# Optimization experiments

Measured on AMD Instinct MI355X. Metric: run time of the kernel, lower is better.

Reference implementation:

```python
import jax, jax.numpy as jnp
import numpy as np

N_NODES = 100000
N_EDGES = 1600000


def gcn_conv(x, W, b, src, dst, ew, n):
    """PyG GCNConv: x@W, symmetric deg^-1/2 norm with self-loops, scatter-add at dst, +b."""
    loop = jnp.arange(n, dtype=src.dtype)
    s = jnp.concatenate([src, loop])            # sources incl. self-loops
    d = jnp.concatenate([dst, loop])            # targets incl. self-loops
    w = jnp.concatenate([ew, jnp.ones((n,), ew.dtype)])  # self-loop weight = 1
    deg = jax.ops.segment_sum(w, d, num_segments=n)      # weighted in-degree
    dinv = jnp.where(deg > 0, jax.lax.rsqrt(deg), 0.0)
    norm = dinv[s] * w * dinv[d]                # [E+N]
    h = x @ W                                   # [N, F_out]
    msg = h[s] * norm[:, None]                  # gather + per-edge scale
    out = jax.ops.segment_sum(msg, d, num_segments=n)    # scatter-add
    return out + b


def setup_inputs() -> dict:
    key = jax.random.key(0)
    ks = jax.random.split(key, 8)
    in_dim, hid, lat = 128, 128, 64
    x = jax.random.normal(ks[0], (N_NODES, in_dim), jnp.float32)
    edge_index = jax.random.randint(ks[1], (2, N_EDGES), 0, N_NODES, dtype=jnp.int32)
    weights = jax.random.uniform(ks[2], (N_EDGES,), jnp.float32)
    s_in = 1.0 / np.sqrt(in_dim)
    s_h = 1.0 / np.sqrt(hid)
    return {
        "x": x,
        "edge_index": edge_index,
        "weights": weights,
        "W1": jax.random.normal(ks[3], (in_dim, hid), jnp.float32) * s_in,
        "b1": jnp.zeros((hid,), jnp.float32),
        "W2": jax.random.normal(ks[4], (hid, hid), jnp.float32) * s_h,
        "b2": jnp.zeros((hid,), jnp.float32),
        "W_mu": jax.random.normal(ks[5], (hid, lat), jnp.float32) * s_h,
        "b_mu": jnp.zeros((lat,), jnp.float32),
        "W_lv": jax.random.normal(ks[6], (hid, lat), jnp.float32) * s_h,
        "b_lv": jnp.zeros((lat,), jnp.float32),
    }


def reference(x, edge_index, weights, W1, b1, W2, b2, W_mu, b_mu, W_lv, b_lv):
    n = x.shape[0]
    src, dst = edge_index[0], edge_index[1]
    h = jax.nn.relu(gcn_conv(x, W1, b1, src, dst, weights, n))
    h = gcn_conv(h, W2, b2, src, dst, weights, n)
    g = jnp.mean(h, axis=0, keepdims=True)      # [1, hid] global mean pool
    mu = g @ W_mu + b_mu
    logvar = g @ W_lv + b_lv
    return (mu, logvar)
```

## Files before the change

### kernel.cpp

```cpp
#include <hip/hip_runtime.h>


typedef __bf16 bf16x8 __attribute__((ext_vector_type(8)));
typedef float f32x4 __attribute__((ext_vector_type(4)));
typedef float f32x2 __attribute__((ext_vector_type(2)));
typedef unsigned long long u64;

#define NSL 24

__device__ __forceinline__ float bf2f(unsigned short u){
  return __uint_as_float(((unsigned)u) << 16);
}
__device__ __forceinline__ unsigned short f2bf(float f){
  unsigned u = __float_as_uint(f);
  u += 0x7fffu + ((u >> 16) & 1u);
  return (unsigned short)(u >> 16);
}
__device__ __forceinline__ __bf16 us2bf(unsigned short u){
  __bf16 b; __builtin_memcpy(&b, &u, 2); return b;
}
__device__ __forceinline__ float ldf(const void* p, int i, int isf32){
  return isf32 ? ((const float*)p)[i] : bf2f(((const unsigned short*)p)[i]);
}
__device__ __forceinline__ void fma8f8(float* acc, float n, uint2 h){
  f32x2 p0 = __builtin_amdgcn_cvt_pk_f32_fp8((int)h.x, false);
  f32x2 p1 = __builtin_amdgcn_cvt_pk_f32_fp8((int)h.x, true);
  f32x2 p2 = __builtin_amdgcn_cvt_pk_f32_fp8((int)h.y, false);
  f32x2 p3 = __builtin_amdgcn_cvt_pk_f32_fp8((int)h.y, true);
  acc[0] = fmaf(n, p0[0], acc[0]);
  acc[1] = fmaf(n, p0[1], acc[1]);
  acc[2] = fmaf(n, p1[0], acc[2]);
  acc[3] = fmaf(n, p1[1], acc[3]);
  acc[4] = fmaf(n, p2[0], acc[4]);
  acc[5] = fmaf(n, p2[1], acc[5]);
  acc[6] = fmaf(n, p3[0], acc[6]);
  acc[7] = fmaf(n, p3[1], acc[7]);
}
__device__ __forceinline__ void runOfShard(const int* __restrict__ hist, int r, int s,
                                           int lane, int& off, int& len){
  int hv = (lane < 8) ? hist[r * 8 + lane] : 0;
  off = 0; len = 0;
  #pragma unroll
  for (int i = 0; i < 8; ++i){
    int h = __shfl(hv, i);
    if (i < s) off += h;
    if (i == s) len = h;
  }
}

__global__ void k_init(const unsigned* __restrict__ xw, int* __restrict__ flag,
                       const void* __restrict__ W1, unsigned short* __restrict__ W1T,
                       float* __restrict__ v){
  __shared__ int s[256];
  int t = threadIdx.x;
  int cnt = 0;
  for (int k = t; k < 4096; k += 256){
    unsigned lo = xw[k] & 0xFFFFu;
    int e = (int)((lo >> 7) & 0xFFu);
    if ((e >= 100 && e <= 141) || (lo & 0x7FFFu) == 0) cnt++;
  }
  s[t] = cnt;
  __syncthreads();
  for (int off = 128; off > 0; off >>= 1){
    if (t < off) s[t] += s[t + off];
    __syncthreads();
  }
  int isf32 = (s[0] < 2458) ? 1 : 0;
  if (blockIdx.x == 0){
    if (t == 0) *flag = isf32;
    if (t < 128) v[t] = 0.0f;
  }
  int gid = blockIdx.x * 256 + t;
  int k = gid & 127, n = gid >> 7;
  W1T[gid] = isf32 ? f2bf(((const float*)W1)[k * 128 + n])
                   : ((const unsigned short*)W1)[k * 128 + n];
}

__global__ void __launch_bounds__(256) k_binA(const int* __restrict__ src,
    const int* __restrict__ dst, const void* __restrict__ w,
    u64* __restrict__ stagD, u64* __restrict__ stagS,
    int* __restrict__ histD, int* __restrict__ histS,
    int E, int DSv, const int* __restrict__ flagp){
  __shared__ int gcnt[256];
  __shared__ int gincl[256];
  __shared__ u64 bufD[1024];
  __shared__ u64 bufS[1024];
  int tid = threadIdx.x, lane = tid & 63, wv = tid >> 6;
  gcnt[tid] = 0;
  __syncthreads();
  int isf32 = *flagp;
  u64 ltmask = (1ull << lane) - 1ull;
  int sh1v[4], off1v[4], sh2v[4], off2v[4];
  u64 r1v[4], r2v[4];
  #pragma unroll
  for (int k = 0; k < 4; ++k){
    int e = blockIdx.x * 1024 + k * 256 + tid;
    int sh1 = -1, sh2 = -1; u64 r1 = 0, r2 = 0;
    if (e < E){
      int s_ = src[e], d_ = dst[e];
      float wf = ldf(w, e, isf32);
      int nq = (int)(wf * 32768.0f + 0.5f);
      if (nq > 32767) nq = 32767;
      r1 = ((u64)(unsigned)d_ << 32) | ((u64)(unsigned)s_ << 15) | (unsigned)nq;
      r2 = ((u64)(unsigned)s_ << 32) | ((u64)(unsigned)d_ << 15) | (unsigned)nq;
      sh1 = d_ / DSv;
      sh2 = s_ / DSv;
    }
    int o1 = 0, o2 = 0;
    #pragma unroll
    for (int s = 0; s < 8; ++s){
      u64 m1 = __ballot(sh1 == s);
      if (sh1 == s){ o1 = __popcll(m1 & ltmask); if (!o1) gcnt[s * 16 + k * 4 + wv] = __popcll(m1); }
      u64 m2 = __ballot(sh2 == s);
      if (sh2 == s){ o2 = __popcll(m2 & ltmask); if (!o2) gcnt[128 + s * 16 + k * 4 + wv] = __popcll(m2); }
    }
    sh1v[k] = sh1; off1v[k] = o1; r1v[k] = r1;
    sh2v[k] = sh2; off2v[k] = o2; r2v[k] = r2;
  }
  __syncthreads();
  gincl[tid] = gcnt[tid];
  __syncthreads();
  for (int ofs = 1; ofs < 256; ofs <<= 1){
    int t2 = (tid >= ofs) ? gincl[tid - ofs] : 0;
    __syncthreads();
    gincl[tid] += t2;
    __syncthreads();
  }
  int tot1 = gincl[127];
  #pragma unroll
  for (int k = 0; k < 4; ++k){
    if (sh1v[k] >= 0){
      int i1 = sh1v[k] * 16 + k * 4 + wv;
      bufD[gincl[i1] - gcnt[i1] + off1v[k]] = r1v[k];
      int i2 = 128 + sh2v[k] * 16 + k * 4 + wv;
      bufS[gincl[i2] - gcnt[i2] - tot1 + off2v[k]] = r2v[k];
    }
  }
  __syncthreads();
  for (int t = tid; t < tot1; t += 256)
    stagD[(size_t)blockIdx.x * 1024 + t] = bufD[t];
  int tot2 = gincl[255] - tot1;
  for (int t = tid; t < tot2; t += 256)
    stagS[(size_t)blockIdx.x * 1024 + t] = bufS[t];
  if (tid < 8){
    int a  = gincl[tid * 16 + 15];
    int pr = tid ? gincl[tid * 16 - 1] : 0;
    histD[blockIdx.x * 8 + tid] = a - pr;
    int a2  = gincl[128 + tid * 16 + 15];
    int pr2 = gincl[128 + tid * 16 - 1];
    histS[blockIdx.x * 8 + tid] = a2 - pr2;
  }
}

__global__ void __launch_bounds__(256) k_binB(const u64* __restrict__ stagD,
    const int* __restrict__ histD, unsigned* __restrict__ cntdegP,
    int NREG, int per, int DSv){
  __shared__ unsigned cd[12512];
  int tid = threadIdx.x, lane = tid & 63, wv = tid >> 6;
  int s = (int)blockIdx.x & 7, j = (int)blockIdx.x >> 3;
  for (int i = tid; i < DSv; i += 256) cd[i] = 0u;
  __syncthreads();
  int r0 = j * per, r1 = r0 + per;
  if (r1 > NREG) r1 = NREG;
  for (int r = r0 + wv; r < r1; r += 4){
    int off, len;
    runOfShard(histD, r, s, lane, off, len);
    const u64* rp = stagD + (size_t)r * 1024 + off;
    for (int i = lane; i < len; i += 64){
      u64 rec = rp[i];
      int dl = (int)(rec >> 32) - s * DSv;
      if ((unsigned)dl < (unsigned)DSv)
        atomicAdd(&cd[dl], (1u << 20) | (unsigned)((rec & 32767u) >> 2));
    }
  }
  __syncthreads();
  unsigned* op = cntdegP + (size_t)blockIdx.x * DSv;
  for (int i = tid; i < DSv; i += 256) op[i] = cd[i];
}

__global__ void k_scanA(const unsigned* __restrict__ cntdegP, float* __restrict__ dinv,
                        int* __restrict__ cnt, int* __restrict__ rowptr,
                        int* __restrict__ bsum, int N, int DSv){
  __shared__ int sm[256];
  int i = blockIdx.x * 256 + threadIdx.x;
  int val = 0;
  if (i < N){
    int s = i / DSv, local = i - s * DSv;
    unsigned c = 0, dg = 0;
    #pragma unroll
    for (int j = 0; j < NSL; ++j){
      unsigned p = cntdegP[(size_t)(j * 8 + s) * DSv + local];
      c += p >> 20;
      dg += p & 0xFFFFFu;
    }
    dinv[i] = rsqrtf(1.0f + (float)dg * (1.0f / 8192.0f));
    cnt[i] = (int)c;
    val = (int)c;
  }
  sm[threadIdx.x] = val;
  __syncthreads();
  for (int off = 1; off < 256; off <<= 1){
    int tmp = (threadIdx.x >= off) ? sm[threadIdx.x - off] : 0;
    __syncthreads();
    sm[threadIdx.x] += tmp;
    __syncthreads();
  }
  if (i < N) rowptr[i] = sm[threadIdx.x] - val;
  if (threadIdx.x == 255) bsum[blockIdx.x] = sm[255];
}

__global__ void k_scanB(const int* __restrict__ bsum, int* __restrict__ boffs, int NB){
  __shared__ int s[512];
  int t = threadIdx.x;
  int val = (t < NB) ? bsum[t] : 0;
  s[t] = val;
  __syncthreads();
  for (int off = 1; off < 512; off <<= 1){
    int tmp = (t >= off) ? s[t - off] : 0;
    __syncthreads();
    s[t] += tmp;
    __syncthreads();
  }
  boffs[t] = s[t] - val;
}

__global__ void k_scanC(int* __restrict__ rowptr, const int* __restrict__ boffs,
                        const unsigned* __restrict__ cntdegP, int* __restrict__ P,
                        int N, int DSv){
  int i = blockIdx.x * 256 + threadIdx.x;
  if (i >= N) return;
  int rp = rowptr[i] + boffs[blockIdx.x];
  rowptr[i] = rp;
  int s = i / DSv, local = i - s * DSv;
  int run = rp;
  #pragma unroll
  for (int j = 0; j < NSL; ++j){
    P[(size_t)j * N + i] = run;
    run += (int)(cntdegP[(size_t)(j * 8 + s) * DSv + local] >> 20);
  }
}

__global__ void __launch_bounds__(256) k_binC(const u64* __restrict__ stagD,
    const int* __restrict__ histD, const int* __restrict__ P,
    const float* __restrict__ dinv, unsigned* __restrict__ edges,
    int NREG, int per, int N, int DSv, int E){
  __shared__ unsigned cur[12512];
  int tid = threadIdx.x, lane = tid & 63, wv = tid >> 6;
  int s = (int)blockIdx.x & 7, j = (int)blockIdx.x >> 3;
  for (int i = tid; i < DSv; i += 256){
    int node = s * DSv + i;
    cur[i] = (node < N) ? (unsigned)P[(size_t)j * N + node] : 0u;
  }
  __syncthreads();
  int r0 = j * per, r1 = r0 + per;
  if (r1 > NREG) r1 = NREG;
  for (int r = r0 + wv; r < r1; r += 4){
    int off, len;
    runOfShard(histD, r, s, lane, off, len);
    const u64* rp = stagD + (size_t)r * 1024 + off;
    for (int i = lane; i < len; i += 64){
      u64 rec = rp[i];
      int dl = (int)(rec >> 32) - s * DSv;
      if ((unsigned)dl < (unsigned)DSv){
        int srcI = (int)((rec >> 15) & 0x1FFFFu);
        float nrm = dinv[srcI] * ((float)(rec & 32767u) * (1.0f / 32768.0f))
                  * dinv[s * DSv + dl];
        int nq = (int)(nrm * 32768.0f + 0.5f);
        if (nq > 32767) nq = 32767;
        unsigned pos = atomicAdd(&cur[dl], 1u);
        if (pos < (unsigned)E) edges[pos] = ((unsigned)srcI << 15) | (unsigned)nq;
      }
    }
  }
}

__global__ void __launch_bounds__(256) k_cfacB(const u64* __restrict__ stagS,
    const int* __restrict__ histS, const float* __restrict__ dinv,
    float* __restrict__ cfacP, int NREG, int per, int DSv){
  __shared__ float SL[12512];
  int tid = threadIdx.x, lane = tid & 63, wv = tid >> 6;
  int s = (int)blockIdx.x & 7, j = (int)blockIdx.x >> 3;
  for (int i = tid; i < DSv; i += 256) SL[i] = 0.0f;
  __syncthreads();
  int r0 = j * per, r1 = r0 + per;
  if (r1 > NREG) r1 = NREG;
  for (int r = r0 + wv; r < r1; r += 4){
    int off, len;
    runOfShard(histS, r, s, lane, off, len);
    const u64* rp = stagS + (size_t)r * 1024 + off;
    for (int i = lane; i < len; i += 64){
      u64 rec = rp[i];
      int sl_ = (int)(rec >> 32) - s * DSv;
      int d   = (int)((rec >> 15) & 0x1FFFFu);
      float wq = (float)(rec & 32767u) * (1.0f / 32768.0f);
      if ((unsigned)sl_ < (unsigned)DSv)
        atomicAdd(&SL[sl_], wq * dinv[d]);
    }
  }
  __syncthreads();
  float* op = cfacP + (size_t)blockIdx.x * DSv;
  for (int i = tid; i < DSv; i += 256) op[i] = SL[i];
}

__global__ void k_cfacm(const float* __restrict__ cfacP, const float* __restrict__ dinv,
                        const int* __restrict__ rowptr, const int* __restrict__ cnt,
                        float2* __restrict__ dc, int2* __restrict__ rc,
                        unsigned* __restrict__ edges, int E, int N, int DSv){
  if (blockIdx.x == 0 && threadIdx.x < 16) edges[E + threadIdx.x] = 0u;
  int i = blockIdx.x * 256 + threadIdx.x;
  if (i >= N) return;
  int s = i / DSv, ii = i - s * DSv;
  float S = 0.0f;
  #pragma unroll
  for (int j = 0; j < NSL; ++j)
    S += cfacP[(size_t)(j * 8 + s) * DSv + ii];
  float di = dinv[i];
  dc[i] = make_float2(di * di, di * di + di * S);
  rc[i] = make_int2(rowptr[i], cnt[i]);
}

__global__ void __launch_bounds__(256) k_gemm(const void* __restrict__ xv,
                                              const __bf16* __restrict__ wt,
                                              unsigned char* __restrict__ H, int N,
                                              const int* __restrict__ flagp){
  int wave = (blockIdx.x * blockDim.x + threadIdx.x) >> 6;
  int lane = threadIdx.x & 63;
  int row16 = wave << 4;
  if (row16 >= N) return;
  int isf32 = *flagp;
  int m = lane & 15, q = lane >> 4;
  bf16x8 a0, a1, a2, a3;
  if (isf32){
    const float* ap = (const float*)xv + (size_t)(row16 + m) * 128 + q * 8;
    #pragma unroll
    for (int j = 0; j < 8; ++j){
      a0[j] = us2bf(f2bf(ap[j +  0]));
      a1[j] = us2bf(f2bf(ap[j + 32]));
      a2[j] = us2bf(f2bf(ap[j + 64]));
      a3[j] = us2bf(f2bf(ap[j + 96]));
    }
  } else {
    const __bf16* ap = (const __bf16*)xv + (size_t)(row16 + m) * 128 + q * 8;
    a0 = *(const bf16x8*)(ap +  0);
    a1 = *(const bf16x8*)(ap + 32);
    a2 = *(const bf16x8*)(ap + 64);
    a3 = *(const bf16x8*)(ap + 96);
  }
  for (int nt = 0; nt < 8; ++nt){
    const __bf16* bp = wt + (size_t)(nt * 16 + m) * 128 + q * 8;
    bf16x8 b0 = *(const bf16x8*)(bp +  0);
    bf16x8 b1 = *(const bf16x8*)(bp + 32);
    bf16x8 b2 = *(const bf16x8*)(bp + 64);
    bf16x8 b3 = *(const bf16x8*)(bp + 96);
    f32x4 acc = {0.f, 0.f, 0.f, 0.f};
    acc = __builtin_amdgcn_mfma_f32_16x16x32_bf16(a0, b0, acc, 0, 0, 0);
    acc = __builtin_amdgcn_mfma_f32_16x16x32_bf16(a1, b1, acc, 0, 0, 0);
    acc = __builtin_amdgcn_mfma_f32_16x16x32_bf16(a2, b2, acc, 0, 0, 0);
    acc = __builtin_amdgcn_mfma_f32_16x16x32_bf16(a3, b3, acc, 0, 0, 0);
    unsigned char* op = H + (size_t)(row16 + q * 4) * 128 + nt * 16 + m;
    op[0]   = (unsigned char)(__builtin_amdgcn_cvt_pk_fp8_f32(acc[0], acc[0], 0, false) & 0xFF);
    op[128] = (unsigned char)(__builtin_amdgcn_cvt_pk_fp8_f32(acc[1], acc[1], 0, false) & 0xFF);
    op[256] = (unsigned char)(__builtin_amdgcn_cvt_pk_fp8_f32(acc[2], acc[2], 0, false) & 0xFF);
    op[384] = (unsigned char)(__builtin_amdgcn_cvt_pk_fp8_f32(acc[3], acc[3], 0, false) & 0xFF);
  }
}

__global__ void __launch_bounds__(256) k_agg(const unsigned char* __restrict__ H,
    const int2* __restrict__ rc, const float2* __restrict__ dc,
    const unsigned* __restrict__ edges, const void* __restrict__ b1,
    float* __restrict__ v, int N, int totslots, const int* __restrict__ flagp){
  __shared__ float vsh[128];
  __shared__ float bsh[128];
  int tid = threadIdx.x;
  int isf32 = *flagp;
  if (tid < 128){ vsh[tid] = 0.0f; bsh[tid] = ldf(b1, tid, isf32); }
  __syncthreads();
  int lane = tid & 63;
  int wv = tid >> 6;
  int slot = lane >> 3;
  int q = lane & 7;
  int slotg = ((int)blockIdx.x * 4 + wv) * 8 + slot;
  const unsigned char* Hq = H + q * 16;
  float ax[16];
  #pragma unroll
  for (int j = 0; j < 16; ++j) ax[j] = 0.0f;
  int d = slotg;
  int2 rcv = make_int2(0, 0); float2 dcv = make_float2(0.f, 0.f);
  uint4 hs = make_uint4(0u, 0u, 0u, 0u);
  if (d < N){
    rcv = rc[d]; dcv = dc[d];
    hs = *(const uint4*)(Hq + (size_t)d * 128);
  }
  while (d < N){
    int dn = d + totslots;
    int2 rcn = make_int2(0, 0); float2 dcn = make_float2(0.f, 0.f);
    uint4 hsn = make_uint4(0u, 0u, 0u, 0u);
    if (dn < N){
      rcn = rc[dn]; dcn = dc[dn];
      hsn = *(const uint4*)(Hq + (size_t)dn * 128);
    }
    float acc[16];
    #pragma unroll
    for (int j = 0; j < 16; ++j) acc[j] = 0.0f;
    fma8f8(acc,     dcv.x, make_uint2(hs.x, hs.y));
    fma8f8(acc + 8, dcv.x, make_uint2(hs.z, hs.w));
    int start = rcv.x, len = rcv.y;
    if (len > 0){
      const unsigned* ep = edges + start;
      unsigned e0 = ep[0], e1 = ep[1], e2 = ep[2], e3 = ep[3];
      uint4 h0 = *(const uint4*)(Hq + (size_t)(e0 >> 15) * 128);
      uint4 h1 = *(const uint4*)(Hq + (size_t)(e1 >> 15) * 128);
      uint4 h2 = *(const uint4*)(Hq + (size_t)(e2 >> 15) * 128);
      #pragma unroll 2
      for (int k = 0; k < len; ++k){
        unsigned en = ep[k + 4];
        uint4 hn = *(const uint4*)(Hq + (size_t)(e3 >> 15) * 128);
        float wn = (float)(e0 & 32767u) * (1.0f / 32768.0f);
        fma8f8(acc,     wn, make_uint2(h0.x, h0.y));
        fma8f8(acc + 8, wn, make_uint2(h0.z, h0.w));
        e0 = e1; e1 = e2; e2 = e3; e3 = en;
        h0 = h1; h1 = h2; h2 = hn;
      }
    }
    #pragma unroll
    for (int j = 0; j < 16; ++j){
      float rj = fmaxf(acc[j] + bsh[q * 16 + j], 0.0f);
      ax[j] = fmaf(dcv.y, rj, ax[j]);
    }
    d = dn; rcv = rcn; dcv = dcn; hs = hsn;
  }
  #pragma unroll
  for (int j = 0; j < 16; ++j){
    ax[j] += __shfl_xor(ax[j], 8);
    ax[j] += __shfl_xor(ax[j], 16);
    ax[j] += __shfl_xor(ax[j], 32);
  }
  if (slot == 0){
    #pragma unroll
    for (int j = 0; j < 16; ++j) atomicAdd(&vsh[q * 16 + j], ax[j]);
  }
  __syncthreads();
  if (tid < 128) atomicAdd(&v[tid], vsh[tid]);
}

__global__ void __launch_bounds__(128) k_head(const float* __restrict__ v,
    const void* __restrict__ W2, const void* __restrict__ b2,
    const void* __restrict__ Wmu, const void* __restrict__ bmu,
    const void* __restrict__ Wlv, const void* __restrict__ blv,
    void* __restrict__ outv, float invN, const int* __restrict__ flagp){
  __shared__ float gsh[128];
  __shared__ float tsh[128];
  int t = threadIdx.x;
  int isf32 = *flagp;
  gsh[t] = v[t] * invN;
  __syncthreads();
  float acc = ldf(b2, t, isf32);
  for (int k = 0; k < 128; ++k) acc = fmaf(gsh[k], ldf(W2, k * 128 + t, isf32), acc);
  tsh[t] = acc;
  __syncthreads();
  int j = t & 63;
  const void* Wp = (t < 64) ? Wmu : Wlv;
  float o = ldf((t < 64) ? bmu : blv, j, isf32);
  for (int k = 0; k < 128; ++k) o = fmaf(tsh[k], ldf(Wp, k * 64 + j, isf32), o);
  if (isf32) ((float*)outv)[t] = o;
  else       ((unsigned short*)outv)[t] = f2bf(o);
}

extern "C" void kernel_launch(void* const* d_in, const int* in_sizes, int n_in,
                              void* d_out, int out_size, void* d_ws, size_t ws_size,
                              hipStream_t stream) {
  const void* x   = d_in[0];
  const int*  ei  = (const int*)d_in[1];
  const void* w   = d_in[2];
  const void* W1  = d_in[3];
  const void* b1  = d_in[4];
  const void* W2  = d_in[5];
  const void* b2  = d_in[6];
  const void* Wmu = d_in[7];
  const void* bmu = d_in[8];
  const void* Wlv = d_in[9];
  const void* blv = d_in[10];

  const int N = in_sizes[0] / 128;
  const int E = in_sizes[2];
  const int* src = ei;
  const int* dst = ei + E;

  char* wsb = (char*)d_ws;
  size_t off = 0;
  auto alloc = [&](size_t bytes) -> void* {
    off = (off + 255) & ~(size_t)255;
    void* p = wsb + off;
    off += bytes;
    return p;
  };
  const int NREG = (E + 1023) / 1024;
  const int PER  = (NREG + NSL - 1) / NSL;
  const int DSv  = (N + 7) / 8;
  int*   flag     = (int*)  alloc(16);
  float* dinv     = (float*)alloc((size_t)N * 4);
  int*   cnt      = (int*)  alloc((size_t)N * 4);
  int*   rowptr   = (int*)  alloc((size_t)(N + 1) * 4);
  float2* dc      = (float2*)alloc((size_t)N * 8);
  int2*   rc      = (int2*) alloc((size_t)N * 8);
  int*   bsum     = (int*)  alloc(512 * 4);
  int*   boffs    = (int*)  alloc(512 * 4);
  float* v        = (float*)alloc(128 * 4);
  int*   histD    = (int*)  alloc((size_t)NREG * 8 * 4);
  int*   histS    = (int*)  alloc((size_t)NREG * 8 * 4);
  unsigned short* W1T = (unsigned short*)alloc(128 * 128 * 2);
  size_t P_b = (size_t)NSL * N * 4, cfacP_b = (size_t)NSL * 8 * DSv * 4;
  char* regionP = (char*)alloc(P_b > cfacP_b ? P_b : cfacP_b);
  int*   P     = (int*)regionP;
  float* cfacP = (float*)regionP;
  size_t cdg_b = (size_t)NSL * 8 * DSv * 4, edges_b = (size_t)E * 4 + 64;
  char* regionE = (char*)alloc(cdg_b > edges_b ? cdg_b : edges_b);
  unsigned* cntdegP = (unsigned*)regionE;
  unsigned* edges   = (unsigned*)regionE;
  size_t stagD_b = (size_t)NREG * 1024 * 8, H_b = (size_t)N * 128;
  char* regionD = (char*)alloc(stagD_b > H_b ? stagD_b : H_b);
  u64*           stagD = (u64*)regionD;
  unsigned char* H     = (unsigned char*)regionD;
  u64* stagS = (u64*)alloc((size_t)NREG * 1024 * 8);
  (void)ws_size; (void)n_in; (void)out_size;

  const int nb_n = (N + 255) / 256;

  k_init<<<64, 256, 0, stream>>>((const unsigned*)x, flag, W1, W1T, v);
  k_binA<<<NREG, 256, 0, stream>>>(src, dst, w, stagD, stagS, histD, histS,
                                   E, DSv, flag);
  k_binB<<<NSL * 8, 256, 0, stream>>>(stagD, histD, cntdegP, NREG, PER, DSv);
  k_scanA<<<nb_n, 256, 0, stream>>>(cntdegP, dinv, cnt, rowptr, bsum, N, DSv);
  k_scanB<<<1, 512, 0, stream>>>(bsum, boffs, nb_n);
  k_scanC<<<nb_n, 256, 0, stream>>>(rowptr, boffs, cntdegP, P, N, DSv);
  k_binC<<<NSL * 8, 256, 0, stream>>>(stagD, histD, P, dinv, edges,
                                      NREG, PER, N, DSv, E);
  k_cfacB<<<NSL * 8, 256, 0, stream>>>(stagS, histS, dinv, cfacP, NREG, PER, DSv);
  k_cfacm<<<nb_n, 256, 0, stream>>>(cfacP, dinv, rowptr, cnt, dc, rc,
                                    edges, E, N, DSv);
  const int nwaves = (N + 15) / 16;
  const int nb_g = (nwaves + 3) / 4;
  k_gemm<<<nb_g, 256, 0, stream>>>(x, (const __bf16*)W1T, H, N, flag);
  const int nb_agg = 1024;
  k_agg<<<nb_agg, 256, 0, stream>>>(H, rc, dc, edges, b1, v, N, nb_agg * 32, flag);
  k_head<<<1, 128, 0, stream>>>(v, W2, b2, Wmu, bmu, Wlv, blv,
                                d_out, 1.0f / (float)N, flag);
}
```

Measured before the change: 374.6 us.

## Replace shard-binned CSR build with direct global-atomic degree and edge scatter

Drops the multi-pass staging pipeline (per-block shard binning, LDS-histogram partial counts, per-slice prefix offsets) and builds the CSR with plain global atomics. One 64-bit atomic per edge packs the count and the quantized weighted degree, and a second kernel places each edge with an atomic cursor and accumulates the source-side column factor with a float atomic. This removes several kernels and large staging buffers. In exchange it relies on contended global atomics with random access, and the order of edges within a row becomes nondeterministic.

```diff
diff --git a/kernel.cpp b/kernel.cpp
--- a/kernel.cpp
+++ b/kernel.cpp
@@ -5,8 +5,6 @@
 typedef float f32x4 __attribute__((ext_vector_type(4)));
 typedef float f32x2 __attribute__((ext_vector_type(2)));
 typedef unsigned long long u64;
-
-#define NSL 24
 
 __device__ __forceinline__ float bf2f(unsigned short u){
   return __uint_as_float(((unsigned)u) << 16);
@@ -36,21 +34,10 @@
   acc[6] = fmaf(n, p3[0], acc[6]);
   acc[7] = fmaf(n, p3[1], acc[7]);
 }
-__device__ __forceinline__ void runOfShard(const int* __restrict__ hist, int r, int s,
-                                           int lane, int& off, int& len){
-  int hv = (lane < 8) ? hist[r * 8 + lane] : 0;
-  off = 0; len = 0;
-  #pragma unroll
-  for (int i = 0; i < 8; ++i){
-    int h = __shfl(hv, i);
-    if (i < s) off += h;
-    if (i == s) len = h;
-  }
-}
 
 __global__ void k_init(const unsigned* __restrict__ xw, int* __restrict__ flag,
                        const void* __restrict__ W1, unsigned short* __restrict__ W1T,
-                       float* __restrict__ v){
+                       float* __restrict__ v, u64* __restrict__ degcnt, int N){
   __shared__ int s[256];
   int t = threadIdx.x;
   int cnt = 0;
@@ -71,131 +58,39 @@
     if (t < 128) v[t] = 0.0f;
   }
   int gid = blockIdx.x * 256 + t;
+  for (int i = gid; i < N; i += 16384) degcnt[i] = 0ull;
   int k = gid & 127, n = gid >> 7;
   W1T[gid] = isf32 ? f2bf(((const float*)W1)[k * 128 + n])
                    : ((const unsigned short*)W1)[k * 128 + n];
 }
 
-__global__ void __launch_bounds__(256) k_binA(const int* __restrict__ src,
-    const int* __restrict__ dst, const void* __restrict__ w,
-    u64* __restrict__ stagD, u64* __restrict__ stagS,
-    int* __restrict__ histD, int* __restrict__ histS,
-    int E, int DSv, const int* __restrict__ flagp){
-  __shared__ int gcnt[256];
-  __shared__ int gincl[256];
-  __shared__ u64 bufD[1024];
-  __shared__ u64 bufS[1024];
-  int tid = threadIdx.x, lane = tid & 63, wv = tid >> 6;
-  gcnt[tid] = 0;
-  __syncthreads();
-  int isf32 = *flagp;
-  u64 ltmask = (1ull << lane) - 1ull;
-  int sh1v[4], off1v[4], sh2v[4], off2v[4];
-  u64 r1v[4], r2v[4];
-  #pragma unroll
-  for (int k = 0; k < 4; ++k){
-    int e = blockIdx.x * 1024 + k * 256 + tid;
-    int sh1 = -1, sh2 = -1; u64 r1 = 0, r2 = 0;
-    if (e < E){
-      int s_ = src[e], d_ = dst[e];
-      float wf = ldf(w, e, isf32);
-      int nq = (int)(wf * 32768.0f + 0.5f);
-      if (nq > 32767) nq = 32767;
-      r1 = ((u64)(unsigned)d_ << 32) | ((u64)(unsigned)s_ << 15) | (unsigned)nq;
-      r2 = ((u64)(unsigned)s_ << 32) | ((u64)(unsigned)d_ << 15) | (unsigned)nq;
-      sh1 = d_ / DSv;
-      sh2 = s_ / DSv;
-    }
-    int o1 = 0, o2 = 0;
-    #pragma unroll
-    for (int s = 0; s < 8; ++s){
-      u64 m1 = __ballot(sh1 == s);
-      if (sh1 == s){ o1 = __popcll(m1 & ltmask); if (!o1) gcnt[s * 16 + k * 4 + wv] = __popcll(m1); }
-      u64 m2 = __ballot(sh2 == s);
-      if (sh2 == s){ o2 = __popcll(m2 & ltmask); if (!o2) gcnt[128 + s * 16 + k * 4 + wv] = __popcll(m2); }
-    }
-    sh1v[k] = sh1; off1v[k] = o1; r1v[k] = r1;
-    sh2v[k] = sh2; off2v[k] = o2; r2v[k] = r2;
-  }
-  __syncthreads();
-  gincl[tid] = gcnt[tid];
-  __syncthreads();
-  for (int ofs = 1; ofs < 256; ofs <<= 1){
-    int t2 = (tid >= ofs) ? gincl[tid - ofs] : 0;
-    __syncthreads();
-    gincl[tid] += t2;
-    __syncthreads();
-  }
-  int tot1 = gincl[127];
-  #pragma unroll
-  for (int k = 0; k < 4; ++k){
-    if (sh1v[k] >= 0){
-      int i1 = sh1v[k] * 16 + k * 4 + wv;
-      bufD[gincl[i1] - gcnt[i1] + off1v[k]] = r1v[k];
-      int i2 = 128 + sh2v[k] * 16 + k * 4 + wv;
-      bufS[gincl[i2] - gcnt[i2] - tot1 + off2v[k]] = r2v[k];
-    }
-  }
-  __syncthreads();
-  for (int t = tid; t < tot1; t += 256)
-    stagD[(size_t)blockIdx.x * 1024 + t] = bufD[t];
-  int tot2 = gincl[255] - tot1;
-  for (int t = tid; t < tot2; t += 256)
-    stagS[(size_t)blockIdx.x * 1024 + t] = bufS[t];
-  if (tid < 8){
-    int a  = gincl[tid * 16 + 15];
-    int pr = tid ? gincl[tid * 16 - 1] : 0;
-    histD[blockIdx.x * 8 + tid] = a - pr;
-    int a2  = gincl[128 + tid * 16 + 15];
-    int pr2 = gincl[128 + tid * 16 - 1];
-    histS[blockIdx.x * 8 + tid] = a2 - pr2;
-  }
-}
-
-__global__ void __launch_bounds__(256) k_binB(const u64* __restrict__ stagD,
-    const int* __restrict__ histD, unsigned* __restrict__ cntdegP,
-    int NREG, int per, int DSv){
-  __shared__ unsigned cd[12512];
-  int tid = threadIdx.x, lane = tid & 63, wv = tid >> 6;
-  int s = (int)blockIdx.x & 7, j = (int)blockIdx.x >> 3;
-  for (int i = tid; i < DSv; i += 256) cd[i] = 0u;
-  __syncthreads();
-  int r0 = j * per, r1 = r0 + per;
-  if (r1 > NREG) r1 = NREG;
-  for (int r = r0 + wv; r < r1; r += 4){
-    int off, len;
-    runOfShard(histD, r, s, lane, off, len);
-    const u64* rp = stagD + (size_t)r * 1024 + off;
-    for (int i = lane; i < len; i += 64){
-      u64 rec = rp[i];
-      int dl = (int)(rec >> 32) - s * DSv;
-      if ((unsigned)dl < (unsigned)DSv)
-        atomicAdd(&cd[dl], (1u << 20) | (unsigned)((rec & 32767u) >> 2));
-    }
-  }
-  __syncthreads();
-  unsigned* op = cntdegP + (size_t)blockIdx.x * DSv;
-  for (int i = tid; i < DSv; i += 256) op[i] = cd[i];
-}
-
-__global__ void k_scanA(const unsigned* __restrict__ cntdegP, float* __restrict__ dinv,
+__global__ void __launch_bounds__(256) k_deg(const int* __restrict__ dst,
+    const void* __restrict__ w, u64* __restrict__ degcnt, int E,
+    const int* __restrict__ flagp){
+  int isf32 = *flagp;
+  int e = blockIdx.x * 256 + threadIdx.x;
+  if (e >= E) return;
+  int d_ = dst[e];
+  float wf = ldf(w, e, isf32);
+  int nq = (int)(wf * 32768.0f + 0.5f);
+  if (nq > 32767) nq = 32767;
+  atomicAdd(&degcnt[d_], (1ull << 40) | (u64)(unsigned)(nq >> 2));
+}
+
+__global__ void k_scanA(const u64* __restrict__ degcnt, float* __restrict__ dinv,
                         int* __restrict__ cnt, int* __restrict__ rowptr,
-                        int* __restrict__ bsum, int N, int DSv){
+                        int* __restrict__ bsum, float* __restrict__ S, int N){
   __shared__ int sm[256];
   int i = blockIdx.x * 256 + threadIdx.x;
   int val = 0;
   if (i < N){
-    int s = i / DSv, local = i - s * DSv;
-    unsigned c = 0, dg = 0;
-    #pragma unroll
-    for (int j = 0; j < NSL; ++j){
-      unsigned p = cntdegP[(size_t)(j * 8 + s) * DSv + local];
-      c += p >> 20;
-      dg += p & 0xFFFFFu;
-    }
+    u64 p = degcnt[i];
+    u64 dg = p & ((1ull << 40) - 1ull);
+    int c = (int)(p >> 40);
     dinv[i] = rsqrtf(1.0f + (float)dg * (1.0f / 8192.0f));
-    cnt[i] = (int)c;
-    val = (int)c;
+    cnt[i] = c;
+    val = c;
+    S[i] = 0.0f;
   }
   sm[threadIdx.x] = val;
   __syncthreads();
@@ -225,97 +120,45 @@
 }
 
 __global__ void k_scanC(int* __restrict__ rowptr, const int* __restrict__ boffs,
-                        const unsigned* __restrict__ cntdegP, int* __restrict__ P,
-                        int N, int DSv){
+                        unsigned* __restrict__ cur, int N){
   int i = blockIdx.x * 256 + threadIdx.x;
   if (i >= N) return;
   int rp = rowptr[i] + boffs[blockIdx.x];
   rowptr[i] = rp;
-  int s = i / DSv, local = i - s * DSv;
-  int run = rp;
-  #pragma unroll
-  for (int j = 0; j < NSL; ++j){
-    P[(size_t)j * N + i] = run;
-    run += (int)(cntdegP[(size_t)(j * 8 + s) * DSv + local] >> 20);
-  }
-}
-
-__global__ void __launch_bounds__(256) k_binC(const u64* __restrict__ stagD,
-    const int* __restrict__ histD, const int* __restrict__ P,
-    const float* __restrict__ dinv, unsigned* __restrict__ edges,
-    int NREG, int per, int N, int DSv, int E){
-  __shared__ unsigned cur[12512];
-  int tid = threadIdx.x, lane = tid & 63, wv = tid >> 6;
-  int s = (int)blockIdx.x & 7, j = (int)blockIdx.x >> 3;
-  for (int i = tid; i < DSv; i += 256){
-    int node = s * DSv + i;
-    cur[i] = (node < N) ? (unsigned)P[(size_t)j * N + node] : 0u;
-  }
-  __syncthreads();
-  int r0 = j * per, r1 = r0 + per;
-  if (r1 > NREG) r1 = NREG;
-  for (int r = r0 + wv; r < r1; r += 4){
-    int off, len;
-    runOfShard(histD, r, s, lane, off, len);
-    const u64* rp = stagD + (size_t)r * 1024 + off;
-    for (int i = lane; i < len; i += 64){
-      u64 rec = rp[i];
-      int dl = (int)(rec >> 32) - s * DSv;
-      if ((unsigned)dl < (unsigned)DSv){
-        int srcI = (int)((rec >> 15) & 0x1FFFFu);
-        float nrm = dinv[srcI] * ((float)(rec & 32767u) * (1.0f / 32768.0f))
-                  * dinv[s * DSv + dl];
-        int nq = (int)(nrm * 32768.0f + 0.5f);
-        if (nq > 32767) nq = 32767;
-        unsigned pos = atomicAdd(&cur[dl], 1u);
-        if (pos < (unsigned)E) edges[pos] = ((unsigned)srcI << 15) | (unsigned)nq;
-      }
-    }
-  }
-}
-
-__global__ void __launch_bounds__(256) k_cfacB(const u64* __restrict__ stagS,
-    const int* __restrict__ histS, const float* __restrict__ dinv,
-    float* __restrict__ cfacP, int NREG, int per, int DSv){
-  __shared__ float SL[12512];
-  int tid = threadIdx.x, lane = tid & 63, wv = tid >> 6;
-  int s = (int)blockIdx.x & 7, j = (int)blockIdx.x >> 3;
-  for (int i = tid; i < DSv; i += 256) SL[i] = 0.0f;
-  __syncthreads();
-  int r0 = j * per, r1 = r0 + per;
-  if (r1 > NREG) r1 = NREG;
-  for (int r = r0 + wv; r < r1; r += 4){
-    int off, len;
-    runOfShard(histS, r, s, lane, off, len);
-    const u64* rp = stagS + (size_t)r * 1024 + off;
-    for (int i = lane; i < len; i += 64){
-      u64 rec = rp[i];
-      int sl_ = (int)(rec >> 32) - s * DSv;
-      int d   = (int)((rec >> 15) & 0x1FFFFu);
-      float wq = (float)(rec & 32767u) * (1.0f / 32768.0f);
-      if ((unsigned)sl_ < (unsigned)DSv)
-        atomicAdd(&SL[sl_], wq * dinv[d]);
-    }
-  }
-  __syncthreads();
-  float* op = cfacP + (size_t)blockIdx.x * DSv;
-  for (int i = tid; i < DSv; i += 256) op[i] = SL[i];
-}
-
-__global__ void k_cfacm(const float* __restrict__ cfacP, const float* __restrict__ dinv,
+  cur[i] = (unsigned)rp;
+}
+
+__global__ void __launch_bounds__(256) k_edges(const int* __restrict__ src,
+    const int* __restrict__ dst, const void* __restrict__ w,
+    const float* __restrict__ dinv, unsigned* __restrict__ cur,
+    float* __restrict__ S, unsigned* __restrict__ edges, int E,
+    const int* __restrict__ flagp){
+  int isf32 = *flagp;
+  int e = blockIdx.x * 256 + threadIdx.x;
+  if (e >= E) return;
+  int s_ = src[e], d_ = dst[e];
+  float wf = ldf(w, e, isf32);
+  int wq = (int)(wf * 32768.0f + 0.5f);
+  if (wq > 32767) wq = 32767;
+  float wqf = (float)wq * (1.0f / 32768.0f);
+  float dd = dinv[d_];
+  float nrm = dinv[s_] * wqf * dd;
+  int nq = (int)(nrm * 32768.0f + 0.5f);
+  if (nq > 32767) nq = 32767;
+  unsigned pos = atomicAdd(&cur[d_], 1u);
+  edges[pos] = ((unsigned)s_ << 15) | (unsigned)nq;
+  atomicAdd(&S[s_], wqf * dd);
+}
+
+__global__ void k_cfacm(const float* __restrict__ S, const float* __restrict__ dinv,
                         const int* __restrict__ rowptr, const int* __restrict__ cnt,
                         float2* __restrict__ dc, int2* __restrict__ rc,
-                        unsigned* __restrict__ edges, int E, int N, int DSv){
+                        unsigned* __restrict__ edges, int E, int N){
   if (blockIdx.x == 0 && threadIdx.x < 16) edges[E + threadIdx.x] = 0u;
   int i = blockIdx.x * 256 + threadIdx.x;
   if (i >= N) return;
-  int s = i / DSv, ii = i - s * DSv;
-  float S = 0.0f;
-  #pragma unroll
-  for (int j = 0; j < NSL; ++j)
-    S += cfacP[(size_t)(j * 8 + s) * DSv + ii];
   float di = dinv[i];
-  dc[i] = make_float2(di * di, di * di + di * S);
+  dc[i] = make_float2(di * di, di * di + di * S[i]);
   rc[i] = make_int2(rowptr[i], cnt[i]);
 }
 
@@ -379,12 +222,11 @@
   int wv = tid >> 6;
   int slot = lane >> 3;
   int q = lane & 7;
-  int slotg = ((int)blockIdx.x * 4 + wv) * 8 + slot;
   const unsigned char* Hq = H + q * 16;
   float ax[16];
   #pragma unroll
   for (int j = 0; j < 16; ++j) ax[j] = 0.0f;
-  int d = slotg;
+  int d = ((int)blockIdx.x * 4 + wv) * 8 + slot;
   int2 rcv = make_int2(0, 0); float2 dcv = make_float2(0.f, 0.f);
   uint4 hs = make_uint4(0u, 0u, 0u, 0u);
   if (d < N){
@@ -494,9 +336,6 @@
     off += bytes;
     return p;
   };
-  const int NREG = (E + 1023) / 1024;
-  const int PER  = (NREG + NSL - 1) / NSL;
-  const int DSv  = (N + 7) / 8;
   int*   flag     = (int*)  alloc(16);
   float* dinv     = (float*)alloc((size_t)N * 4);
   int*   cnt      = (int*)  alloc((size_t)N * 4);
@@ -506,38 +345,24 @@
   int*   bsum     = (int*)  alloc(512 * 4);
   int*   boffs    = (int*)  alloc(512 * 4);
   float* v        = (float*)alloc(128 * 4);
-  int*   histD    = (int*)  alloc((size_t)NREG * 8 * 4);
-  int*   histS    = (int*)  alloc((size_t)NREG * 8 * 4);
   unsigned short* W1T = (unsigned short*)alloc(128 * 128 * 2);
-  size_t P_b = (size_t)NSL * N * 4, cfacP_b = (size_t)NSL * 8 * DSv * 4;
-  char* regionP = (char*)alloc(P_b > cfacP_b ? P_b : cfacP_b);
-  int*   P     = (int*)regionP;
-  float* cfacP = (float*)regionP;
-  size_t cdg_b = (size_t)NSL * 8 * DSv * 4, edges_b = (size_t)E * 4 + 64;
-  char* regionE = (char*)alloc(cdg_b > edges_b ? cdg_b : edges_b);
-  unsigned* cntdegP = (unsigned*)regionE;
-  unsigned* edges   = (unsigned*)regionE;
-  size_t stagD_b = (size_t)NREG * 1024 * 8, H_b = (size_t)N * 128;
-  char* regionD = (char*)alloc(stagD_b > H_b ? stagD_b : H_b);
-  u64*           stagD = (u64*)regionD;
-  unsigned char* H     = (unsigned char*)regionD;
-  u64* stagS = (u64*)alloc((size_t)NREG * 1024 * 8);
+  u64*      degcnt = (u64*)     alloc((size_t)N * 8);
+  unsigned* cur    = (unsigned*)alloc((size_t)N * 4);
+  float*    S      = (float*)   alloc((size_t)N * 4);
+  unsigned* edges  = (unsigned*)alloc((size_t)E * 4 + 64);
+  unsigned char* H = (unsigned char*)alloc((size_t)N * 128);
   (void)ws_size; (void)n_in; (void)out_size;
 
   const int nb_n = (N + 255) / 256;
-
-  k_init<<<64, 256, 0, stream>>>((const unsigned*)x, flag, W1, W1T, v);
-  k_binA<<<NREG, 256, 0, stream>>>(src, dst, w, stagD, stagS, histD, histS,
-                                   E, DSv, flag);
-  k_binB<<<NSL * 8, 256, 0, stream>>>(stagD, histD, cntdegP, NREG, PER, DSv);
-  k_scanA<<<nb_n, 256, 0, stream>>>(cntdegP, dinv, cnt, rowptr, bsum, N, DSv);
+  const int nb_e = (E + 255) / 256;
+
+  k_init<<<64, 256, 0, stream>>>((const unsigned*)x, flag, W1, W1T, v, degcnt, N);
+  k_deg<<<nb_e, 256, 0, stream>>>(dst, w, degcnt, E, flag);
+  k_scanA<<<nb_n, 256, 0, stream>>>(degcnt, dinv, cnt, rowptr, bsum, S, N);
   k_scanB<<<1, 512, 0, stream>>>(bsum, boffs, nb_n);
-  k_scanC<<<nb_n, 256, 0, stream>>>(rowptr, boffs, cntdegP, P, N, DSv);
-  k_binC<<<NSL * 8, 256, 0, stream>>>(stagD, histD, P, dinv, edges,
-                                      NREG, PER, N, DSv, E);
-  k_cfacB<<<NSL * 8, 256, 0, stream>>>(stagS, histS, dinv, cfacP, NREG, PER, DSv);
-  k_cfacm<<<nb_n, 256, 0, stream>>>(cfacP, dinv, rowptr, cnt, dc, rc,
-                                    edges, E, N, DSv);
+  k_scanC<<<nb_n, 256, 0, stream>>>(rowptr, boffs, cur, N);
+  k_edges<<<nb_e, 256, 0, stream>>>(src, dst, w, dinv, cur, S, edges, E, flag);
+  k_cfacm<<<nb_n, 256, 0, stream>>>(S, dinv, rowptr, cnt, dc, rc, edges, E, N);
   const int nwaves = (N + 15) / 16;
   const int nb_g = (nwaves + 3) / 4;
   k_gemm<<<nb_g, 256, 0, stream>>>(x, (const __bf16*)W1T, H, N, flag);
```

After: 451.4 us. +20.5%, slower.
